# Kernel tuning notes

Measured on AMD Instinct MI355X. Metric: run time of the kernel, lower is better.

## Reference

```python
import jax, jax.numpy as jnp
import numpy as np

B, T, I, H = 1024, 200, 128, 128


def setup_inputs() -> dict:
    key = jax.random.key(0)
    ks = jax.random.split(key, 8)
    s = 1.0 / np.sqrt(I + H)
    return {
        "inputs": jax.random.normal(ks[0], (B, T, I), dtype=jnp.float32),
        "attention_scores": jax.random.uniform(ks[1], (B, T), dtype=jnp.float32),
        "Wz": jax.random.normal(ks[2], (H, I + H), dtype=jnp.float32) * s,
        "bz": jax.random.normal(ks[3], (H,), dtype=jnp.float32) * s,
        "Wr": jax.random.normal(ks[4], (H, I + H), dtype=jnp.float32) * s,
        "br": jax.random.normal(ks[5], (H,), dtype=jnp.float32) * s,
        "Wh": jax.random.normal(ks[6], (H, I + H), dtype=jnp.float32) * s,
        "bh": jax.random.normal(ks[7], (H,), dtype=jnp.float32) * s,
    }


def reference(inputs, attention_scores, Wz, bz, Wr, br, Wh, bh):
    b, t, i = inputs.shape
    h_dim = Wz.shape[0]
    # Split each gate weight into its x-part and h-part:
    # linear(cat(x, h)) == x @ Wx.T + h @ Wh_.T + b
    Wz_x, Wz_h = Wz[:, :i], Wz[:, i:]
    Wr_x, Wr_h = Wr[:, :i], Wr[:, i:]
    Wh_x, Wh_h = Wh[:, :i], Wh[:, i:]

    # Precompute input projections in one batched GEMM each: [T, B, H]
    xz = jnp.einsum('bti,hi->tbh', inputs, Wz_x) + bz
    xr = jnp.einsum('bti,hi->tbh', inputs, Wr_x) + br
    xh = jnp.einsum('bti,hi->tbh', inputs, Wh_x) + bh
    a = attention_scores.T  # [T, B]

    h0 = jnp.zeros((b, h_dim), dtype=inputs.dtype)

    def step(h, xs):
        xz_t, xr_t, xh_t, a_t = xs
        z = jax.nn.sigmoid(xz_t + h @ Wz_h.T)
        r = jax.nn.sigmoid(xr_t + h @ Wr_h.T)
        h_tilde = jnp.tanh(xh_t + (r * h) @ Wh_h.T)
        z_prime = a_t[:, None] * z
        h_new = (1.0 - z_prime) * h + z_prime * h_tilde
        return h_new, None

    h_final, _ = jax.lax.scan(step, h0, (xz, xr, xh, a))
    return h_final
```

## Files before the change

### kernel.cpp

```cpp
#include <hip/hip_runtime.h>


#define T_N   200
#define I_DIM 128
#define H_DIM 128
#define NBLK  64
#define TCHUNK 25

typedef float  f32x4  __attribute__((ext_vector_type(4)));
typedef __bf16 bf16x4 __attribute__((ext_vector_type(4)));
typedef __bf16 bf16x8 __attribute__((ext_vector_type(8)));

#define GATE_BYTES 4096
#define PB_BYTES   (3 * GATE_BYTES)
#define PRE_BYTES  ((size_t)T_N * NBLK * PB_BYTES)

#define LDA_STRIDE 264
#define LATT_STRIDE 201

__device__ __forceinline__ float fast_sigmoid(float x) {
  float e = __builtin_amdgcn_exp2f(-1.4426950408889634f * x);
  return __builtin_amdgcn_rcpf(1.0f + e);
}
__device__ __forceinline__ float fast_tanh(float x) {
  float e = __builtin_amdgcn_exp2f(2.8853900817779268f * x);
  return 1.0f - 2.0f * __builtin_amdgcn_rcpf(1.0f + e);
}
__device__ __forceinline__ void barrier_lds() {
  asm volatile("s_waitcnt lgkmcnt(0)\n\ts_barrier" ::: "memory");
}
__device__ __forceinline__ bf16x8 pack8(float4 a, float4 b) {
  bf16x8 t;
  t[0] = (__bf16)a.x; t[1] = (__bf16)a.y; t[2] = (__bf16)a.z; t[3] = (__bf16)a.w;
  t[4] = (__bf16)b.x; t[5] = (__bf16)b.y; t[6] = (__bf16)b.z; t[7] = (__bf16)b.w;
  return t;
}
__device__ __forceinline__ int swz(int row, int bytecol) {
  return row * 256 + (bytecol ^ ((row & 7) << 4));
}

__global__ __launch_bounds__(256, 2)
void xproj_kernel(const float* __restrict__ inputs,
                  const float* __restrict__ Wz, const float* __restrict__ bz,
                  const float* __restrict__ Wr, const float* __restrict__ br,
                  const float* __restrict__ Wh, const float* __restrict__ bh,
                  char* __restrict__ pre) {
  __shared__ __align__(16) char lds_x[2 * 4096];

  const int tid  = threadIdx.x;
  const int w    = tid >> 6;
  const int l    = tid & 63;
  const int l15  = l & 15;
  const int lk   = l >> 4;
  const int bblk = blockIdx.x & (NBLK - 1);
  const int t0   = (blockIdx.x >> 6) * TCHUNK;
  const int r0   = bblk * 16;

  const int crow  = tid >> 4;
  const int cslot = tid & 15;
  const float* xsrc = inputs + (size_t)(r0 + crow) * (T_N * I_DIM) + cslot * 8;
  const int cwoff = swz(crow, cslot * 16);

  bf16x8 wb[24];
  f32x4  bias4[6];
  #pragma unroll
  for (int s = 0; s < 6; ++s) {
    int hid0 = w * 32 + (s & 1) * 16;
    const float* Wp; const float* bp;
    if (s < 2)      { Wp = Wz; bp = bz; }
    else if (s < 4) { Wp = Wr; bp = br; }
    else            { Wp = Wh; bp = bh; }
    float4 bv = *(const float4*)&bp[hid0 + lk * 4];
    bias4[s][0] = bv.x; bias4[s][1] = bv.y; bias4[s][2] = bv.z; bias4[s][3] = bv.w;
    const float* Wrow = Wp + (size_t)(hid0 + l15) * 256;
    #pragma unroll
    for (int kt = 0; kt < 4; ++kt) {
      const float* p = Wrow + kt * 32 + lk * 8;
      wb[s * 4 + kt] = pack8(*(const float4*)p, *(const float4*)(p + 4));
    }
  }

  {
    const float* p = xsrc + (size_t)t0 * I_DIM;
    float4 a = *(const float4*)p;
    float4 b = *(const float4*)(p + 4);
    *(bf16x8*)(lds_x + cwoff) = pack8(a, b);
  }
  barrier_lds();

  #pragma unroll 2
  for (int ti = 0; ti < TCHUNK; ++ti) {
    const int t = t0 + ti;
    float4 ra, rb2;
    if (ti + 1 < TCHUNK) {
      const float* p = xsrc + (size_t)(t + 1) * I_DIM;
      ra  = *(const float4*)p;
      rb2 = *(const float4*)(p + 4);
    }

    char* bufc = lds_x + ((ti & 1) ? 4096 : 0);
    bf16x8 xf[4];
    #pragma unroll
    for (int kt = 0; kt < 4; ++kt)
      xf[kt] = *(const bf16x8*)(bufc + swz(l15, kt * 64 + lk * 16));

    f32x4 acc[6];
    #pragma unroll
    for (int s = 0; s < 6; ++s) acc[s] = bias4[s];
    #pragma unroll
    for (int kt = 0; kt < 4; ++kt)
      #pragma unroll
      for (int s = 0; s < 6; ++s)
        acc[s] = __builtin_amdgcn_mfma_f32_16x16x32_bf16(wb[s * 4 + kt], xf[kt], acc[s], 0, 0, 0);

    char* base = pre + ((size_t)t * NBLK + bblk) * PB_BYTES;
    #pragma unroll
    for (int s = 0; s < 6; ++s) {
      int g      = s >> 1;
      int hidgrp = w * 8 + (s & 1) * 4 + lk;
      bf16x4 v;
      v[0] = (__bf16)acc[s][0]; v[1] = (__bf16)acc[s][1];
      v[2] = (__bf16)acc[s][2]; v[3] = (__bf16)acc[s][3];
      *(bf16x4*)(base + g * GATE_BYTES + hidgrp * 128 + l15 * 8) = v;
    }

    if (ti + 1 < TCHUNK) {
      char* bufn = lds_x + (((ti + 1) & 1) ? 4096 : 0);
      *(bf16x8*)(bufn + cwoff) = pack8(ra, rb2);
    }
    barrier_lds();
  }
}

__global__ __launch_bounds__(512, 1)
void augru_rec_kernel(const char* __restrict__ pre,
                      const float* __restrict__ attn,
                      const float* __restrict__ Wz,
                      const float* __restrict__ Wr,
                      const float* __restrict__ Wh,
                      float* __restrict__ out) {
  __shared__ __align__(16) short lds_h [16 * 128];
  __shared__ __align__(16) short lds_rh[16 * 128];
  __shared__ float lds_att[T_N * 16];

  const int tid   = threadIdx.x;
  const int w     = tid >> 6;
  const int l     = tid & 63;
  const int l15   = l & 15;
  const int lk    = l >> 4;
  const int r0    = blockIdx.x * 16;
  const int myhid = w * 16 + lk * 4;

  for (int idx = tid; idx < T_N * 16; idx += 512) {
    int t = idx >> 4, b = idx & 15;
    lds_att[idx] = attn[(size_t)(r0 + b) * T_N + t];
  }
  for (int idx = tid; idx < 16 * 128; idx += 512) lds_h[idx] = 0;

  bf16x8 wzH[4], wrH[4], whH[4];
  {
    const float* pz = Wz + (size_t)(w * 16 + l15) * 256 + 128;
    const float* pr = Wr + (size_t)(w * 16 + l15) * 256 + 128;
    const float* ph = Wh + (size_t)(w * 16 + l15) * 256 + 128;
    #pragma unroll
    for (int kt = 0; kt < 4; ++kt) {
      const float* a = pz + kt * 32 + lk * 8;
      wzH[kt] = pack8(*(const float4*)a, *(const float4*)(a + 4));
      const float* b = pr + kt * 32 + lk * 8;
      wrH[kt] = pack8(*(const float4*)b, *(const float4*)(b + 4));
      const float* cc = ph + kt * 32 + lk * 8;
      whH[kt] = pack8(*(const float4*)cc, *(const float4*)(cc + 4));
    }
  }

  float hreg[4];
  #pragma unroll
  for (int q = 0; q < 4; ++q) hreg[q] = 0.0f;

  const char* pb = pre + (size_t)blockIdx.x * PB_BYTES + (w * 4 + lk) * 128 + l15 * 8;
  const size_t tstride = (size_t)NBLK * PB_BYTES;
  bf16x4 pf[2][3];
  #pragma unroll
  for (int d = 0; d < 2; ++d)
    #pragma unroll
    for (int g = 0; g < 3; ++g)
      pf[d][g] = *(const bf16x4*)(pb + d * tstride + g * GATE_BYTES);

  const int wr_off = swz(l15, 32 * w + 8 * lk);

  __syncthreads();

  #pragma unroll 2
  for (int t = 0; t < T_N; ++t) {
    float pzv[4], prv[4], phv[4];
    #pragma unroll
    for (int q = 0; q < 4; ++q) {
      pzv[q] = (float)pf[t & 1][0][q];
      prv[q] = (float)pf[t & 1][1][q];
      phv[q] = (float)pf[t & 1][2][q];
    }
    if (t + 2 < T_N) {
      const char* b = pb + (size_t)(t + 2) * tstride;
      #pragma unroll
      for (int g = 0; g < 3; ++g)
        pf[t & 1][g] = *(const bf16x4*)(b + g * GATE_BYTES);
    }

    bf16x8 hb[4];
    #pragma unroll
    for (int kt = 0; kt < 4; ++kt)
      hb[kt] = *(const bf16x8*)((const char*)lds_h + swz(l15, kt * 64 + lk * 16));
    const float av = lds_att[t * 16 + l15];

    f32x4 zA, zB, rA, rB;
    { f32x4 a; a[0]=pzv[0]; a[1]=pzv[1]; a[2]=pzv[2]; a[3]=pzv[3]; zA = a; }
    { f32x4 a; a[0]=prv[0]; a[1]=prv[1]; a[2]=prv[2]; a[3]=prv[3]; rA = a; }
    { f32x4 z; z[0]=0.f; z[1]=0.f; z[2]=0.f; z[3]=0.f; zB = z; rB = z; }
    zA = __builtin_amdgcn_mfma_f32_16x16x32_bf16(wzH[0], hb[0], zA, 0, 0, 0);
    rA = __builtin_amdgcn_mfma_f32_16x16x32_bf16(wrH[0], hb[0], rA, 0, 0, 0);
    zB = __builtin_amdgcn_mfma_f32_16x16x32_bf16(wzH[1], hb[1], zB, 0, 0, 0);
    rB = __builtin_amdgcn_mfma_f32_16x16x32_bf16(wrH[1], hb[1], rB, 0, 0, 0);
    zA = __builtin_amdgcn_mfma_f32_16x16x32_bf16(wzH[2], hb[2], zA, 0, 0, 0);
    rA = __builtin_amdgcn_mfma_f32_16x16x32_bf16(wrH[2], hb[2], rA, 0, 0, 0);
    zB = __builtin_amdgcn_mfma_f32_16x16x32_bf16(wzH[3], hb[3], zB, 0, 0, 0);
    rB = __builtin_amdgcn_mfma_f32_16x16x32_bf16(wrH[3], hb[3], rB, 0, 0, 0);

    bf16x4 rhv;
    #pragma unroll
    for (int q = 0; q < 4; ++q) {
      float rr = fast_sigmoid(rA[q] + rB[q]);
      rhv[q] = (__bf16)(rr * hreg[q]);
    }
    *(bf16x4*)((char*)lds_rh + wr_off) = rhv;
    float zp[4];
    #pragma unroll
    for (int q = 0; q < 4; ++q)
      zp[q] = av * fast_sigmoid(zA[q] + zB[q]);
    barrier_lds();

    bf16x8 rb[4];
    #pragma unroll
    for (int kt = 0; kt < 4; ++kt)
      rb[kt] = *(const bf16x8*)((const char*)lds_rh + swz(l15, kt * 64 + lk * 16));
    f32x4 hA, hB;
    { f32x4 a; a[0]=phv[0]; a[1]=phv[1]; a[2]=phv[2]; a[3]=phv[3]; hA = a; }
    { f32x4 z; z[0]=0.f; z[1]=0.f; z[2]=0.f; z[3]=0.f; hB = z; }
    hA = __builtin_amdgcn_mfma_f32_16x16x32_bf16(whH[0], rb[0], hA, 0, 0, 0);
    hB = __builtin_amdgcn_mfma_f32_16x16x32_bf16(whH[1], rb[1], hB, 0, 0, 0);
    hA = __builtin_amdgcn_mfma_f32_16x16x32_bf16(whH[2], rb[2], hA, 0, 0, 0);
    hB = __builtin_amdgcn_mfma_f32_16x16x32_bf16(whH[3], rb[3], hB, 0, 0, 0);

    bf16x4 hbv;
    #pragma unroll
    for (int q = 0; q < 4; ++q) {
      float ht = fast_tanh(hA[q] + hB[q]);
      float hn = __builtin_fmaf(zp[q], ht - hreg[q], hreg[q]);
      hreg[q] = hn;
      hbv[q] = (__bf16)hn;
    }
    *(bf16x4*)((char*)lds_h + wr_off) = hbv;
    barrier_lds();
  }

  float4 o;
  o.x = hreg[0]; o.y = hreg[1]; o.z = hreg[2]; o.w = hreg[3];
  *(float4*)&out[(size_t)(r0 + l15) * H_DIM + myhid] = o;
}

__global__ __launch_bounds__(256, 1)
void augru_kernel(const float* __restrict__ inputs,
                  const float* __restrict__ attn,
                  const float* __restrict__ Wz, const float* __restrict__ bz,
                  const float* __restrict__ Wr, const float* __restrict__ br,
                  const float* __restrict__ Wh, const float* __restrict__ bh,
                  float* __restrict__ out) {
  __shared__ __align__(16) short lds_a[16 * LDA_STRIDE];
  __shared__ float lds_att[16 * LATT_STRIDE];

  const int tid = threadIdx.x;
  const int w   = tid >> 6;
  const int l   = tid & 63;
  const int l15 = l & 15;
  const int lk  = l >> 4;
  const int r0  = blockIdx.x * 16;

  for (int idx = tid; idx < 16 * T_N; idx += 256) {
    int row = idx / T_N, t = idx - row * T_N;
    lds_att[row * LATT_STRIDE + t] = attn[(size_t)(r0 + row) * T_N + t];
  }
  for (int idx = tid; idx < 16 * H_DIM; idx += 256) {
    int row = idx >> 7, c = idx & 127;
    lds_a[row * LDA_STRIDE + c] = 0;
  }

  bf16x8 w1[32];
  float  bias1[4];
  #pragma unroll
  for (int ct = 0; ct < 4; ++ct) {
    int n = w * 32 + (ct & 1) * 16 + l15;
    const float* Wp; float bv;
    if (ct < 2) { Wp = Wz + (size_t)n * 256; bv = bz[n]; }
    else        { Wp = Wr + (size_t)n * 256; bv = br[n]; }
    bias1[ct] = bv;
    #pragma unroll
    for (int kt = 0; kt < 8; ++kt) {
      const float* p = Wp + kt * 32 + lk * 8;
      w1[ct * 8 + kt] = pack8(*(const float4*)p, *(const float4*)(p + 4));
    }
  }
  bf16x8 w2[16];
  float  bias2[2];
  #pragma unroll
  for (int ct = 0; ct < 2; ++ct) {
    int n = w * 32 + ct * 16 + l15;
    bias2[ct] = bh[n];
    const float* Wp = Wh + (size_t)n * 256;
    #pragma unroll
    for (int kt = 0; kt < 8; ++kt) {
      const float* p = Wp + kt * 32 + lk * 8;
      w2[ct * 8 + kt] = pack8(*(const float4*)p, *(const float4*)(p + 4));
    }
  }

  float hreg[2][4];
  #pragma unroll
  for (int ct = 0; ct < 2; ++ct)
    #pragma unroll
    for (int q = 0; q < 4; ++q) hreg[ct][q] = 0.0f;

  const float* xbase = inputs + (size_t)(r0 + l15) * (T_N * I_DIM);
  bf16x8 xfrag[4];
  #pragma unroll
  for (int kt = 0; kt < 4; ++kt) {
    const float* p = xbase + kt * 32 + lk * 8;
    xfrag[kt] = pack8(*(const float4*)p, *(const float4*)(p + 4));
  }

  __syncthreads();

  float4 xr0[4], xr1[4];
  for (int t = 0; t < T_N; ++t) {
    if (t + 1 < T_N) {
      #pragma unroll
      for (int kt = 0; kt < 4; ++kt) {
        const float* p = xbase + (size_t)(t + 1) * I_DIM + kt * 32 + lk * 8;
        xr0[kt] = *(const float4*)p;
        xr1[kt] = *(const float4*)(p + 4);
      }
    }
    bf16x8 hfrag[4];
    #pragma unroll
    for (int kt = 0; kt < 4; ++kt)
      hfrag[kt] = *(const bf16x8*)&lds_a[l15 * LDA_STRIDE + kt * 32 + lk * 8];
    float av[4];
    #pragma unroll
    for (int q = 0; q < 4; ++q) av[q] = lds_att[(lk * 4 + q) * LATT_STRIDE + t];

    f32x4 acc[4];
    #pragma unroll
    for (int ct = 0; ct < 4; ++ct) {
      f32x4 a; a[0] = bias1[ct]; a[1] = bias1[ct]; a[2] = bias1[ct]; a[3] = bias1[ct];
      acc[ct] = a;
    }
    #pragma unroll
    for (int kt = 0; kt < 4; ++kt)
      #pragma unroll
      for (int ct = 0; ct < 4; ++ct)
        acc[ct] = __builtin_amdgcn_mfma_f32_16x16x32_bf16(xfrag[kt], w1[ct * 8 + kt], acc[ct], 0, 0, 0);

    f32x4 acc2[2];
    #pragma unroll
    for (int ct = 0; ct < 2; ++ct) {
      f32x4 a; a[0] = bias2[ct]; a[1] = bias2[ct]; a[2] = bias2[ct]; a[3] = bias2[ct];
      acc2[ct] = a;
    }
    #pragma unroll
    for (int kt = 0; kt < 4; ++kt)
      #pragma unroll
      for (int ct = 0; ct < 2; ++ct)
        acc2[ct] = __builtin_amdgcn_mfma_f32_16x16x32_bf16(xfrag[kt], w2[ct * 8 + kt], acc2[ct], 0, 0, 0);

    #pragma unroll
    for (int kt = 0; kt < 4; ++kt)
      #pragma unroll
      for (int ct = 0; ct < 4; ++ct)
        acc[ct] = __builtin_amdgcn_mfma_f32_16x16x32_bf16(hfrag[kt], w1[ct * 8 + 4 + kt], acc[ct], 0, 0, 0);

    float zp[2][4];
    #pragma unroll
    for (int ct = 0; ct < 2; ++ct) {
      int col = w * 32 + ct * 16 + l15;
      #pragma unroll
      for (int q = 0; q < 4; ++q) {
        int row = lk * 4 + q;
        zp[ct][q] = av[q] * fast_sigmoid(acc[ct][q]);
        float rr = fast_sigmoid(acc[2 + ct][q]);
        __bf16 rhb = (__bf16)(rr * hreg[ct][q]);
        lds_a[row * LDA_STRIDE + 128 + col] = __builtin_bit_cast(short, rhb);
      }
    }
    barrier_lds();

    bf16x8 rfrag[4];
    #pragma unroll
    for (int kt = 0; kt < 4; ++kt)
      rfrag[kt] = *(const bf16x8*)&lds_a[l15 * LDA_STRIDE + 128 + kt * 32 + lk * 8];
    #pragma unroll
    for (int kt = 0; kt < 4; ++kt)
      #pragma unroll
      for (int ct = 0; ct < 2; ++ct)
        acc2[ct] = __builtin_amdgcn_mfma_f32_16x16x32_bf16(rfrag[kt], w2[ct * 8 + 4 + kt], acc2[ct], 0, 0, 0);

    if (t + 1 < T_N) {
      #pragma unroll
      for (int kt = 0; kt < 4; ++kt)
        xfrag[kt] = pack8(xr0[kt], xr1[kt]);
    }

    #pragma unroll
    for (int ct = 0; ct < 2; ++ct) {
      int col = w * 32 + ct * 16 + l15;
      #pragma unroll
      for (int q = 0; q < 4; ++q) {
        int row = lk * 4 + q;
        float ht = fast_tanh(acc2[ct][q]);
        float ho = hreg[ct][q];
        float hn = __builtin_fmaf(zp[ct][q], ht - ho, ho);
        hreg[ct][q] = hn;
        __bf16 hb = (__bf16)hn;
        lds_a[row * LDA_STRIDE + col] = __builtin_bit_cast(short, hb);
      }
    }
    barrier_lds();
  }

  #pragma unroll
  for (int ct = 0; ct < 2; ++ct) {
    int col = w * 32 + ct * 16 + l15;
    #pragma unroll
    for (int q = 0; q < 4; ++q) {
      int row = lk * 4 + q;
      out[(size_t)(r0 + row) * H_DIM + col] = hreg[ct][q];
    }
  }
}

extern "C" void kernel_launch(void* const* d_in, const int* in_sizes, int n_in,
                              void* d_out, int out_size, void* d_ws, size_t ws_size,
                              hipStream_t stream) {
  (void)in_sizes; (void)n_in; (void)out_size;
  const float* inputs = (const float*)d_in[0];
  const float* attn   = (const float*)d_in[1];
  const float* Wz     = (const float*)d_in[2];
  const float* bz     = (const float*)d_in[3];
  const float* Wr     = (const float*)d_in[4];
  const float* br     = (const float*)d_in[5];
  const float* Wh     = (const float*)d_in[6];
  const float* bh     = (const float*)d_in[7];
  float* out = (float*)d_out;

  if (ws_size >= PRE_BYTES) {
    char* pre = (char*)d_ws;
    xproj_kernel<<<NBLK * (T_N / TCHUNK), 256, 0, stream>>>(inputs, Wz, bz, Wr, br, Wh, bh, pre);
    augru_rec_kernel<<<NBLK, 512, 0, stream>>>(pre, attn, Wz, Wr, Wh, out);
  } else {
    augru_kernel<<<NBLK, 256, 0, stream>>>(inputs, attn, Wz, bz, Wr, br, Wh, bh, out);
  }
}
```

Before: 236.0 us.

## Split recurrent kernel across 256 blocks of 4 batch rows each

The recurrent kernel now runs 256 blocks, each owning 4 batch rows instead of 16. The MFMA tiles stay 16 wide, so 12 of the 16 columns carry stale or zero data and their results are discarded through the wr_ok guard. The aim is to spread the latency-bound sequential scan over more compute units, at the cost of wasted MFMA work per block. The LDS is also enlarged to an 84 KB static buffer, apparently to force one block per CU.

```diff
diff --git a/kernel.cpp b/kernel.cpp
--- a/kernel.cpp
+++ b/kernel.cpp
@@ -5,6 +5,7 @@
 #define I_DIM 128
 #define H_DIM 128
 #define NBLK  64
+#define NRBLK 256
 #define TCHUNK 25
 
 typedef float  f32x4  __attribute__((ext_vector_type(4)));
@@ -139,20 +140,26 @@
                       const float* __restrict__ Wr,
                       const float* __restrict__ Wh,
                       float* __restrict__ out) {
-  __shared__ __align__(16) short lds_h [16 * 128];
-  __shared__ __align__(16) short lds_rh[16 * 128];
-  __shared__ float lds_att[T_N * 16];
+  __shared__ __align__(16) char lds_all[86016];
+  short* lds_h   = (short*)lds_all;
+  short* lds_rh  = (short*)(lds_all + 4096);
+  float* lds_att = (float*)(lds_all + 8192);
 
   const int tid   = threadIdx.x;
   const int w     = tid >> 6;
   const int l     = tid & 63;
   const int l15   = l & 15;
+  const int l3    = l & 3;
   const int lk    = l >> 4;
-  const int r0    = blockIdx.x * 16;
+  const int rb    = blockIdx.x;
+  const int bblk  = rb >> 2;
+  const int sb    = (rb & 3) * 4;
+  const int r0    = rb * 4;
   const int myhid = w * 16 + lk * 4;
-
-  for (int idx = tid; idx < T_N * 16; idx += 512) {
-    int t = idx >> 4, b = idx & 15;
+  const bool wr_ok = (l15 < 4);
+
+  for (int idx = tid; idx < T_N * 4; idx += 512) {
+    int t = idx >> 2, b = idx & 3;
     lds_att[idx] = attn[(size_t)(r0 + b) * T_N + t];
   }
   for (int idx = tid; idx < 16 * 128; idx += 512) lds_h[idx] = 0;
@@ -177,7 +184,7 @@
   #pragma unroll
   for (int q = 0; q < 4; ++q) hreg[q] = 0.0f;
 
-  const char* pb = pre + (size_t)blockIdx.x * PB_BYTES + (w * 4 + lk) * 128 + l15 * 8;
+  const char* pb = pre + (size_t)bblk * PB_BYTES + (w * 4 + lk) * 128 + (sb + l3) * 8;
   const size_t tstride = (size_t)NBLK * PB_BYTES;
   bf16x4 pf[2][3];
   #pragma unroll
@@ -210,7 +217,7 @@
     #pragma unroll
     for (int kt = 0; kt < 4; ++kt)
       hb[kt] = *(const bf16x8*)((const char*)lds_h + swz(l15, kt * 64 + lk * 16));
-    const float av = lds_att[t * 16 + l15];
+    const float av = lds_att[t * 4 + l3];
 
     f32x4 zA, zB, rA, rB;
     { f32x4 a; a[0]=pzv[0]; a[1]=pzv[1]; a[2]=pzv[2]; a[3]=pzv[3]; zA = a; }
@@ -231,24 +238,24 @@
       float rr = fast_sigmoid(rA[q] + rB[q]);
       rhv[q] = (__bf16)(rr * hreg[q]);
     }
-    *(bf16x4*)((char*)lds_rh + wr_off) = rhv;
+    if (wr_ok) *(bf16x4*)((char*)lds_rh + wr_off) = rhv;
     float zp[4];
     #pragma unroll
     for (int q = 0; q < 4; ++q)
       zp[q] = av * fast_sigmoid(zA[q] + zB[q]);
     barrier_lds();
 
-    bf16x8 rb[4];
-    #pragma unroll
-    for (int kt = 0; kt < 4; ++kt)
-      rb[kt] = *(const bf16x8*)((const char*)lds_rh + swz(l15, kt * 64 + lk * 16));
+    bf16x8 rb4[4];
+    #pragma unroll
+    for (int kt = 0; kt < 4; ++kt)
+      rb4[kt] = *(const bf16x8*)((const char*)lds_rh + swz(l15, kt * 64 + lk * 16));
     f32x4 hA, hB;
     { f32x4 a; a[0]=phv[0]; a[1]=phv[1]; a[2]=phv[2]; a[3]=phv[3]; hA = a; }
     { f32x4 z; z[0]=0.f; z[1]=0.f; z[2]=0.f; z[3]=0.f; hB = z; }
-    hA = __builtin_amdgcn_mfma_f32_16x16x32_bf16(whH[0], rb[0], hA, 0, 0, 0);
-    hB = __builtin_amdgcn_mfma_f32_16x16x32_bf16(whH[1], rb[1], hB, 0, 0, 0);
-    hA = __builtin_amdgcn_mfma_f32_16x16x32_bf16(whH[2], rb[2], hA, 0, 0, 0);
-    hB = __builtin_amdgcn_mfma_f32_16x16x32_bf16(whH[3], rb[3], hB, 0, 0, 0);
+    hA = __builtin_amdgcn_mfma_f32_16x16x32_bf16(whH[0], rb4[0], hA, 0, 0, 0);
+    hB = __builtin_amdgcn_mfma_f32_16x16x32_bf16(whH[1], rb4[1], hB, 0, 0, 0);
+    hA = __builtin_amdgcn_mfma_f32_16x16x32_bf16(whH[2], rb4[2], hA, 0, 0, 0);
+    hB = __builtin_amdgcn_mfma_f32_16x16x32_bf16(whH[3], rb4[3], hB, 0, 0, 0);
 
     bf16x4 hbv;
     #pragma unroll
@@ -258,13 +265,15 @@
       hreg[q] = hn;
       hbv[q] = (__bf16)hn;
     }
-    *(bf16x4*)((char*)lds_h + wr_off) = hbv;
+    if (wr_ok) *(bf16x4*)((char*)lds_h + wr_off) = hbv;
     barrier_lds();
   }
 
-  float4 o;
-  o.x = hreg[0]; o.y = hreg[1]; o.z = hreg[2]; o.w = hreg[3];
-  *(float4*)&out[(size_t)(r0 + l15) * H_DIM + myhid] = o;
+  if (wr_ok) {
+    float4 o;
+    o.x = hreg[0]; o.y = hreg[1]; o.z = hreg[2]; o.w = hreg[3];
+    *(float4*)&out[(size_t)(r0 + l15) * H_DIM + myhid] = o;
+  }
 }
 
 __global__ __launch_bounds__(256, 1)
@@ -462,7 +471,7 @@
   if (ws_size >= PRE_BYTES) {
     char* pre = (char*)d_ws;
     xproj_kernel<<<NBLK * (T_N / TCHUNK), 256, 0, stream>>>(inputs, Wz, bz, Wr, br, Wh, bh, pre);
-    augru_rec_kernel<<<NBLK, 512, 0, stream>>>(pre, attn, Wz, Wr, Wh, out);
+    augru_rec_kernel<<<NRBLK, 512, 0, stream>>>(pre, attn, Wz, Wr, Wh, out);
   } else {
     augru_kernel<<<NBLK, 256, 0, stream>>>(inputs, attn, Wz, bz, Wr, br, Wh, bh, out);
   }
```

After: 230.3 us. 2.4% less time.

## Split z and r gate work across separate wavefronts in recurrent kernel

Applied to the files above, without the earlier changes.

The recurrent kernel now runs 1024 threads per block. Waves 0-7 compute the z gate, the candidate state and the h update, while waves 8-15 compute the r gate and write r*h to LDS. To make that possible, the r waves read h from a new fp32 LDS copy written by the z waves. The aim is to halve the serial MFMA chain per wave in the first phase, at the cost of an extra LDS fp32 store and load each step, more threads synchronizing at each barrier, and idle r waves during the second phase.

```diff
diff --git a/kernel.cpp b/kernel.cpp
--- a/kernel.cpp
+++ b/kernel.cpp
@@ -37,6 +37,9 @@
 }
 __device__ __forceinline__ int swz(int row, int bytecol) {
   return row * 256 + (bytecol ^ ((row & 7) << 4));
+}
+__device__ __forceinline__ int swz32(int row, int bytecol) {
+  return row * 512 + (bytecol ^ ((row & 7) << 4));
 }
 
 __global__ __launch_bounds__(256, 2)
@@ -132,7 +135,7 @@
   }
 }
 
-__global__ __launch_bounds__(512, 1)
+__global__ __launch_bounds__(1024, 1)
 void augru_rec_kernel(const char* __restrict__ pre,
                       const float* __restrict__ attn,
                       const float* __restrict__ Wz,
@@ -141,35 +144,44 @@
                       float* __restrict__ out) {
   __shared__ __align__(16) short lds_h [16 * 128];
   __shared__ __align__(16) short lds_rh[16 * 128];
+  __shared__ __align__(16) float lds_hf[16 * 128];
   __shared__ float lds_att[T_N * 16];
 
-  const int tid   = threadIdx.x;
-  const int w     = tid >> 6;
-  const int l     = tid & 63;
-  const int l15   = l & 15;
-  const int lk    = l >> 4;
-  const int r0    = blockIdx.x * 16;
-  const int myhid = w * 16 + lk * 4;
-
-  for (int idx = tid; idx < T_N * 16; idx += 512) {
+  const int tid  = threadIdx.x;
+  const int w    = tid >> 6;
+  const int l    = tid & 63;
+  const int l15  = l & 15;
+  const int lk   = l >> 4;
+  const int wh   = w & 7;
+  const bool isz = (w < 8);
+  const int r0   = blockIdx.x * 16;
+  const int myhid = wh * 16 + lk * 4;
+
+  for (int idx = tid; idx < T_N * 16; idx += 1024) {
     int t = idx >> 4, b = idx & 15;
     lds_att[idx] = attn[(size_t)(r0 + b) * T_N + t];
   }
-  for (int idx = tid; idx < 16 * 128; idx += 512) lds_h[idx] = 0;
-
-  bf16x8 wzH[4], wrH[4], whH[4];
+  for (int idx = tid; idx < 16 * 128; idx += 1024) {
+    lds_h[idx] = 0;
+    lds_hf[idx] = 0.0f;
+  }
+
+  const float* W1 = isz ? Wz : Wr;
+  bf16x8 w1H[4], whH[4];
   {
-    const float* pz = Wz + (size_t)(w * 16 + l15) * 256 + 128;
-    const float* pr = Wr + (size_t)(w * 16 + l15) * 256 + 128;
-    const float* ph = Wh + (size_t)(w * 16 + l15) * 256 + 128;
+    const float* p1 = W1 + (size_t)(wh * 16 + l15) * 256 + 128;
     #pragma unroll
     for (int kt = 0; kt < 4; ++kt) {
-      const float* a = pz + kt * 32 + lk * 8;
-      wzH[kt] = pack8(*(const float4*)a, *(const float4*)(a + 4));
-      const float* b = pr + kt * 32 + lk * 8;
-      wrH[kt] = pack8(*(const float4*)b, *(const float4*)(b + 4));
-      const float* cc = ph + kt * 32 + lk * 8;
-      whH[kt] = pack8(*(const float4*)cc, *(const float4*)(cc + 4));
+      const float* a = p1 + kt * 32 + lk * 8;
+      w1H[kt] = pack8(*(const float4*)a, *(const float4*)(a + 4));
+    }
+  }
+  if (isz) {
+    const float* p2 = Wh + (size_t)(wh * 16 + l15) * 256 + 128;
+    #pragma unroll
+    for (int kt = 0; kt < 4; ++kt) {
+      const float* a = p2 + kt * 32 + lk * 8;
+      whH[kt] = pack8(*(const float4*)a, *(const float4*)(a + 4));
     }
   }
 
@@ -177,94 +189,101 @@
   #pragma unroll
   for (int q = 0; q < 4; ++q) hreg[q] = 0.0f;
 
-  const char* pb = pre + (size_t)blockIdx.x * PB_BYTES + (w * 4 + lk) * 128 + l15 * 8;
+  const char* pbase = pre + (size_t)blockIdx.x * PB_BYTES + (wh * 4 + lk) * 128 + l15 * 8;
+  const char* pb1 = pbase + (isz ? 0 : GATE_BYTES);
+  const char* pb2 = pbase + 2 * GATE_BYTES;
   const size_t tstride = (size_t)NBLK * PB_BYTES;
-  bf16x4 pf[2][3];
-  #pragma unroll
-  for (int d = 0; d < 2; ++d)
-    #pragma unroll
-    for (int g = 0; g < 3; ++g)
-      pf[d][g] = *(const bf16x4*)(pb + d * tstride + g * GATE_BYTES);
-
-  const int wr_off = swz(l15, 32 * w + 8 * lk);
+  bf16x4 pf1[2], pf2[2];
+  #pragma unroll
+  for (int d = 0; d < 2; ++d) {
+    pf1[d] = *(const bf16x4*)(pb1 + d * tstride);
+    if (isz) pf2[d] = *(const bf16x4*)(pb2 + d * tstride);
+  }
+
+  const int wr_off  = swz(l15, wh * 32 + lk * 8);
+  const int hf_off  = swz32(l15, wh * 64 + lk * 16);
 
   __syncthreads();
 
   #pragma unroll 2
   for (int t = 0; t < T_N; ++t) {
-    float pzv[4], prv[4], phv[4];
-    #pragma unroll
-    for (int q = 0; q < 4; ++q) {
-      pzv[q] = (float)pf[t & 1][0][q];
-      prv[q] = (float)pf[t & 1][1][q];
-      phv[q] = (float)pf[t & 1][2][q];
+    float p1v[4], p2v[4];
+    #pragma unroll
+    for (int q = 0; q < 4; ++q) p1v[q] = (float)pf1[t & 1][q];
+    if (isz) {
+      #pragma unroll
+      for (int q = 0; q < 4; ++q) p2v[q] = (float)pf2[t & 1][q];
     }
     if (t + 2 < T_N) {
-      const char* b = pb + (size_t)(t + 2) * tstride;
-      #pragma unroll
-      for (int g = 0; g < 3; ++g)
-        pf[t & 1][g] = *(const bf16x4*)(b + g * GATE_BYTES);
+      pf1[t & 1] = *(const bf16x4*)(pb1 + (size_t)(t + 2) * tstride);
+      if (isz) pf2[t & 1] = *(const bf16x4*)(pb2 + (size_t)(t + 2) * tstride);
     }
 
     bf16x8 hb[4];
     #pragma unroll
     for (int kt = 0; kt < 4; ++kt)
       hb[kt] = *(const bf16x8*)((const char*)lds_h + swz(l15, kt * 64 + lk * 16));
-    const float av = lds_att[t * 16 + l15];
-
-    f32x4 zA, zB, rA, rB;
-    { f32x4 a; a[0]=pzv[0]; a[1]=pzv[1]; a[2]=pzv[2]; a[3]=pzv[3]; zA = a; }
-    { f32x4 a; a[0]=prv[0]; a[1]=prv[1]; a[2]=prv[2]; a[3]=prv[3]; rA = a; }
-    { f32x4 z; z[0]=0.f; z[1]=0.f; z[2]=0.f; z[3]=0.f; zB = z; rB = z; }
-    zA = __builtin_amdgcn_mfma_f32_16x16x32_bf16(wzH[0], hb[0], zA, 0, 0, 0);
-    rA = __builtin_amdgcn_mfma_f32_16x16x32_bf16(wrH[0], hb[0], rA, 0, 0, 0);
-    zB = __builtin_amdgcn_mfma_f32_16x16x32_bf16(wzH[1], hb[1], zB, 0, 0, 0);
-    rB = __builtin_amdgcn_mfma_f32_16x16x32_bf16(wrH[1], hb[1], rB, 0, 0, 0);
-    zA = __builtin_amdgcn_mfma_f32_16x16x32_bf16(wzH[2], hb[2], zA, 0, 0, 0);
-    rA = __builtin_amdgcn_mfma_f32_16x16x32_bf16(wrH[2], hb[2], rA, 0, 0, 0);
-    zB = __builtin_amdgcn_mfma_f32_16x16x32_bf16(wzH[3], hb[3], zB, 0, 0, 0);
-    rB = __builtin_amdgcn_mfma_f32_16x16x32_bf16(wrH[3], hb[3], rB, 0, 0, 0);
-
-    bf16x4 rhv;
-    #pragma unroll
-    for (int q = 0; q < 4; ++q) {
-      float rr = fast_sigmoid(rA[q] + rB[q]);
-      rhv[q] = (__bf16)(rr * hreg[q]);
-    }
-    *(bf16x4*)((char*)lds_rh + wr_off) = rhv;
+
+    float av = 0.0f;
+    f32x4 hfv;
+    if (isz) av = lds_att[t * 16 + l15];
+    else     hfv = *(const f32x4*)((const char*)lds_hf + hf_off);
+
+    f32x4 a1;
+    a1[0] = p1v[0]; a1[1] = p1v[1]; a1[2] = p1v[2]; a1[3] = p1v[3];
+    a1 = __builtin_amdgcn_mfma_f32_16x16x32_bf16(w1H[0], hb[0], a1, 0, 0, 0);
+    a1 = __builtin_amdgcn_mfma_f32_16x16x32_bf16(w1H[1], hb[1], a1, 0, 0, 0);
+    a1 = __builtin_amdgcn_mfma_f32_16x16x32_bf16(w1H[2], hb[2], a1, 0, 0, 0);
+    a1 = __builtin_amdgcn_mfma_f32_16x16x32_bf16(w1H[3], hb[3], a1, 0, 0, 0);
+
     float zp[4];
-    #pragma unroll
-    for (int q = 0; q < 4; ++q)
-      zp[q] = av * fast_sigmoid(zA[q] + zB[q]);
+    if (isz) {
+      #pragma unroll
+      for (int q = 0; q < 4; ++q) zp[q] = av * fast_sigmoid(a1[q]);
+    } else {
+      bf16x4 rhv;
+      #pragma unroll
+      for (int q = 0; q < 4; ++q) {
+        float rr = fast_sigmoid(a1[q]);
+        rhv[q] = (__bf16)(rr * hfv[q]);
+      }
+      *(bf16x4*)((char*)lds_rh + wr_off) = rhv;
+    }
     barrier_lds();
 
-    bf16x8 rb[4];
-    #pragma unroll
-    for (int kt = 0; kt < 4; ++kt)
-      rb[kt] = *(const bf16x8*)((const char*)lds_rh + swz(l15, kt * 64 + lk * 16));
-    f32x4 hA, hB;
-    { f32x4 a; a[0]=phv[0]; a[1]=phv[1]; a[2]=phv[2]; a[3]=phv[3]; hA = a; }
-    { f32x4 z; z[0]=0.f; z[1]=0.f; z[2]=0.f; z[3]=0.f; hB = z; }
-    hA = __builtin_amdgcn_mfma_f32_16x16x32_bf16(whH[0], rb[0], hA, 0, 0, 0);
-    hB = __builtin_amdgcn_mfma_f32_16x16x32_bf16(whH[1], rb[1], hB, 0, 0, 0);
-    hA = __builtin_amdgcn_mfma_f32_16x16x32_bf16(whH[2], rb[2], hA, 0, 0, 0);
-    hB = __builtin_amdgcn_mfma_f32_16x16x32_bf16(whH[3], rb[3], hB, 0, 0, 0);
-
-    bf16x4 hbv;
-    #pragma unroll
-    for (int q = 0; q < 4; ++q) {
-      float ht = fast_tanh(hA[q] + hB[q]);
-      float hn = __builtin_fmaf(zp[q], ht - hreg[q], hreg[q]);
-      hreg[q] = hn;
-      hbv[q] = (__bf16)hn;
-    }
-    *(bf16x4*)((char*)lds_h + wr_off) = hbv;
+    if (isz) {
+      bf16x8 rb[4];
+      #pragma unroll
+      for (int kt = 0; kt < 4; ++kt)
+        rb[kt] = *(const bf16x8*)((const char*)lds_rh + swz(l15, kt * 64 + lk * 16));
+      f32x4 a2;
+      a2[0] = p2v[0]; a2[1] = p2v[1]; a2[2] = p2v[2]; a2[3] = p2v[3];
+      a2 = __builtin_amdgcn_mfma_f32_16x16x32_bf16(whH[0], rb[0], a2, 0, 0, 0);
+      a2 = __builtin_amdgcn_mfma_f32_16x16x32_bf16(whH[1], rb[1], a2, 0, 0, 0);
+      a2 = __builtin_amdgcn_mfma_f32_16x16x32_bf16(whH[2], rb[2], a2, 0, 0, 0);
+      a2 = __builtin_amdgcn_mfma_f32_16x16x32_bf16(whH[3], rb[3], a2, 0, 0, 0);
+
+      bf16x4 hbv;
+      f32x4  hfw;
+      #pragma unroll
+      for (int q = 0; q < 4; ++q) {
+        float ht = fast_tanh(a2[q]);
+        float hn = __builtin_fmaf(zp[q], ht - hreg[q], hreg[q]);
+        hreg[q] = hn;
+        hbv[q] = (__bf16)hn;
+        hfw[q] = hn;
+      }
+      *(bf16x4*)((char*)lds_h + wr_off) = hbv;
+      *(f32x4*)((char*)lds_hf + hf_off) = hfw;
+    }
     barrier_lds();
   }
 
-  float4 o;
-  o.x = hreg[0]; o.y = hreg[1]; o.z = hreg[2]; o.w = hreg[3];
-  *(float4*)&out[(size_t)(r0 + l15) * H_DIM + myhid] = o;
+  if (isz) {
+    float4 o;
+    o.x = hreg[0]; o.y = hreg[1]; o.z = hreg[2]; o.w = hreg[3];
+    *(float4*)&out[(size_t)(r0 + l15) * H_DIM + myhid] = o;
+  }
 }
 
 __global__ __launch_bounds__(256, 1)
@@ -462,7 +481,7 @@
   if (ws_size >= PRE_BYTES) {
     char* pre = (char*)d_ws;
     xproj_kernel<<<NBLK * (T_N / TCHUNK), 256, 0, stream>>>(inputs, Wz, bz, Wr, br, Wh, bh, pre);
-    augru_rec_kernel<<<NBLK, 512, 0, stream>>>(pre, attn, Wz, Wr, Wh, out);
+    augru_rec_kernel<<<NBLK, 1024, 0, stream>>>(pre, attn, Wz, Wr, Wh, out);
   } else {
     augru_kernel<<<NBLK, 256, 0, stream>>>(inputs, attn, Wz, bz, Wr, br, Wh, bh, out);
   }
```

New measurement: 249.9 us. 5.9% more time.
